# Performance work log

Measured on AMD Instinct MI355X. Metric: run time of the kernel, lower is better.

Reference implementation:

```python
import jax, jax.numpy as jnp
import numpy as np

B, T, D = 4, 4096, 1024
H = 16
DH = D // H
F = 4096
EPS = 1e-5


def _layernorm(x, gamma, beta):
    mu = jnp.mean(x, axis=-1, keepdims=True)
    var = jnp.var(x, axis=-1, keepdims=True)
    return (x - mu) * jax.lax.rsqrt(var + EPS) * gamma + beta


def setup_inputs() -> dict:
    key = jax.random.key(0)
    ks = jax.random.split(key, 10)
    s = 0.02
    return {
        "x": jax.random.normal(ks[0], (B, T, D), dtype=jnp.float32),
        "Wqkv": jax.random.normal(ks[1], (D, 3 * D), dtype=jnp.float32) * s,
        "bqkv": jnp.zeros((3 * D,), dtype=jnp.float32),
        "Wo": jax.random.normal(ks[2], (D, D), dtype=jnp.float32) * s,
        "bo": jnp.zeros((D,), dtype=jnp.float32),
        "W1": jax.random.normal(ks[3], (D, F), dtype=jnp.float32) * s,
        "b1": jnp.zeros((F,), dtype=jnp.float32),
        "W2": jax.random.normal(ks[4], (F, D), dtype=jnp.float32) * s,
        "b2": jnp.zeros((D,), dtype=jnp.float32),
        "g1": jnp.ones((D,), dtype=jnp.float32),
        "be1": jnp.zeros((D,), dtype=jnp.float32),
        "g2": jnp.ones((D,), dtype=jnp.float32),
        "be2": jnp.zeros((D,), dtype=jnp.float32),
    }


def reference(x, Wqkv, bqkv, Wo, bo, W1, b1, W2, b2, g1, be1, g2, be2):
    # fused QKV projection: [B,T,3D]
    qkv = jnp.einsum("btd,de->bte", x, Wqkv) + bqkv
    q, k, v = jnp.split(qkv, 3, axis=-1)
    # [B,H,T,DH]
    q = q.reshape(B, T, H, DH).transpose(0, 2, 1, 3)
    k = k.reshape(B, T, H, DH).transpose(0, 2, 1, 3)
    v = v.reshape(B, T, H, DH).transpose(0, 2, 1, 3)
    scores = jnp.einsum("bhqd,bhkd->bhqk", q, k) / jnp.sqrt(jnp.float32(DH))
    attn = jax.nn.softmax(scores, axis=-1)
    ctx = jnp.einsum("bhqk,bhkd->bhqd", attn, v)
    ctx = ctx.transpose(0, 2, 1, 3).reshape(B, T, D)
    # output projection + residual + post-LN
    x = _layernorm(x + (jnp.einsum("btd,de->bte", ctx, Wo) + bo), g1, be1)
    # FFN (exact GELU, torch default) + residual + post-LN
    h = jax.nn.gelu(jnp.einsum("btd,df->btf", x, W1) + b1, approximate=False)
    ffn = jnp.einsum("btf,fd->btd", h, W2) + b2
    return _layernorm(x + ffn, g2, be2)
```

## Files before the change

kernel.cpp:

```cpp
#include <hip/hip_runtime.h>
#include <math.h>

typedef unsigned short u16;
typedef unsigned int   u32;
typedef __attribute__((ext_vector_type(8))) short short8;
typedef __attribute__((ext_vector_type(4))) float f32x4;

#define B_  4
#define T_  4096
#define D_  1024
#define H_  16
#define DH_ 64
#define F_  4096
#define EPS_ 1e-5f
#define QKV_LD (3 * D_)

#define QSCALE_ 0.18033688011112042f

__device__ __forceinline__ float b2f(u16 v) {
    union { u32 u; float f; } x; x.u = ((u32)v) << 16; return x.f;
}
__device__ __forceinline__ u16 f2b(float f) {
    union { u32 u; float f; } x; x.f = f;
    u32 r = (x.u >> 16) & 1u;
    return (u16)((x.u + 0x7fffu + r) >> 16);
}
__device__ __forceinline__ u16 f2b_fast(float f) {
    union { u32 u; float f; } x; x.f = f;
    return (u16)((x.u + 0x8000u) >> 16);
}

__device__ __forceinline__ float ex2(float x) {
    float r;
    asm("v_exp_f32 %0, %1" : "=v"(r) : "v"(x));
    return r;
}

__device__ __forceinline__ void gll16(const u16* g, u16* ldsbase) {
    __builtin_amdgcn_global_load_lds(
        (const __attribute__((address_space(1))) void*)g,
        (__attribute__((address_space(3))) void*)ldsbase, 16, 0, 0);
}

__global__ __launch_bounds__(256) void conv_bf16_kernel(
    const float* __restrict__ in, u16* __restrict__ out)
{
    const int i = blockIdx.x * 256 + threadIdx.x;
    float4 v = ((const float4*)in)[i];
    ushort4 o;
    o.x = f2b(v.x); o.y = f2b(v.y); o.z = f2b(v.z); o.w = f2b(v.w);
    ((ushort4*)out)[i] = o;
}

__global__ __launch_bounds__(256) void transpose_bf16_kernel(
    const float* __restrict__ W, u16* __restrict__ Wt, int R, int C)
{
    __shared__ float tile[32][33];
    const int bx = blockIdx.x * 32;
    const int by = blockIdx.y * 32;
    const int tx = threadIdx.x & 31, ty = threadIdx.x >> 5;
#pragma unroll
    for (int p = 0; p < 4; ++p)
        tile[ty + p * 8][tx] = W[(size_t)(by + ty + p * 8) * C + bx + tx];
    __syncthreads();
#pragma unroll
    for (int p = 0; p < 4; ++p)
        Wt[(size_t)(bx + ty + p * 8) * R + by + tx] = f2b(tile[tx][ty + p * 8]);
}

template<bool CBF>
__global__ __launch_bounds__(256) void mfma_gemm(
    const u16* __restrict__ A, int lda,
    const u16* __restrict__ Bt, int ldbt,
    const float* __restrict__ bias,
    void* __restrict__ Cv, int ldc,
    int K, int act, int acc, int qcols)
{
    __shared__ __align__(16) u16 Al[128 * 32];
    __shared__ __align__(16) u16 Bl[128 * 32];

    const int tid  = threadIdx.x;
    const int lane = tid & 63, wave = tid >> 6;
    const int quad = lane >> 4, l16 = lane & 15;
    const int m0 = blockIdx.y * 128, n0 = blockIdx.x * 128;
    const int wm = (wave >> 1) * 64, wn = (wave & 1) * 64;

    int srow[2], sgk[2];
#pragma unroll
    for (int t = 0; t < 2; ++t) {
        const int c = wave * 128 + t * 64 + lane;
        srow[t] = c >> 2;
        sgk[t] = ((c & 3) ^ ((srow[t] >> 1) & 3)) * 8;
    }
    const u16* Ag = A  + (size_t)m0 * lda;
    const u16* Bg = Bt + (size_t)n0 * ldbt;
    const int apos = (quad ^ ((l16 >> 1) & 3)) * 8;

    f32x4 accr[4][4];
#pragma unroll
    for (int i = 0; i < 4; ++i)
#pragma unroll
        for (int j = 0; j < 4; ++j)
            accr[i][j] = (f32x4)(0.0f);

    for (int k0 = 0; k0 < K; k0 += 32) {
        __syncthreads();
#pragma unroll
        for (int t = 0; t < 2; ++t) {
            gll16(Ag + (size_t)srow[t] * lda  + k0 + sgk[t], &Al[(wave * 128 + t * 64) * 8]);
            gll16(Bg + (size_t)srow[t] * ldbt + k0 + sgk[t], &Bl[(wave * 128 + t * 64) * 8]);
        }
        __syncthreads();

        short8 af[4], bf[4];
#pragma unroll
        for (int i = 0; i < 4; ++i)
            af[i] = *(const short8*)&Al[(wm + i * 16 + l16) * 32 + apos];
#pragma unroll
        for (int j = 0; j < 4; ++j)
            bf[j] = *(const short8*)&Bl[(wn + j * 16 + l16) * 32 + apos];
#pragma unroll
        for (int i = 0; i < 4; ++i)
#pragma unroll
            for (int j = 0; j < 4; ++j)
                accr[i][j] = __builtin_amdgcn_mfma_f32_16x16x32_bf16(
                    af[i], bf[j], accr[i][j], 0, 0, 0);
    }

#pragma unroll
    for (int j = 0; j < 4; ++j) {
        const int cc = n0 + wn + j * 16 + l16;
        float bv = acc ? 0.0f : bias[cc];
        const float sc = (cc < qcols) ? QSCALE_ : 1.0f;
#pragma unroll
        for (int i = 0; i < 4; ++i) {
#pragma unroll
            for (int r = 0; r < 4; ++r) {
                const int rr = m0 + wm + i * 16 + quad * 4 + r;
                float v = (accr[i][j][r] + bv) * sc;
                if (act == 1)
                    v = 0.5f * v * (1.0f + erff(v * 0.70710678118654752f));
                if (CBF) {
                    ((u16*)Cv)[(size_t)rr * ldc + cc] = f2b(v);
                } else {
                    float* dst = (float*)Cv + (size_t)rr * ldc + cc;
                    if (acc) v += *dst;
                    *dst = v;
                }
            }
        }
    }
}

__global__ __launch_bounds__(256) void attn_mfma_kernel(
    const u16* __restrict__ qkv, u16* __restrict__ ctx)
{
    __shared__ u16 Ks[64 * 72];
    __shared__ u16 Vt[64 * 72];
    __shared__ u16 Ps[4][32 * 72];

    const int tid  = threadIdx.x;
    const int lane = tid & 63, wave = tid >> 6;
    const int quad = lane >> 4, l16 = lane & 15;
    const int b = blockIdx.z, h = blockIdx.y;
    const int q0 = blockIdx.x * 128;

    short8 aq[2][2];
    {
        const u16* qb = qkv + (size_t)(b * T_ + q0 + wave * 32) * QKV_LD + h * DH_;
#pragma unroll
        for (int u = 0; u < 2; ++u)
#pragma unroll
            for (int s = 0; s < 2; ++s)
                aq[u][s] = *(const short8*)(qb + (size_t)(u * 16 + l16) * QKV_LD + s * 32 + quad * 8);
    }

    const int srow = tid >> 3;
    const int scol = (tid & 7) * 8;
    const u16* kg = qkv + (size_t)(b * T_) * QKV_LD + D_     + h * DH_;
    const u16* vg = qkv + (size_t)(b * T_) * QKV_LD + 2 * D_ + h * DH_;

    short8 kreg[2], vreg[2];
#pragma unroll
    for (int half = 0; half < 2; ++half) {
        const int row = srow + half * 32;
        kreg[half] = *(const short8*)(kg + (size_t)row * QKV_LD + scol);
        vreg[half] = *(const short8*)(vg + (size_t)row * QKV_LD + scol);
    }

    f32x4 o_acc[2][4];
#pragma unroll
    for (int u = 0; u < 2; ++u)
#pragma unroll
        for (int nt = 0; nt < 4; ++nt)
            o_acc[u][nt] = (f32x4)(0.0f);
    float l_part[2][4] = {};

    for (int kt = 0; kt < T_; kt += 64) {
        __syncthreads();
#pragma unroll
        for (int half = 0; half < 2; ++half) {
            const int row = srow + half * 32;
            *(short8*)&Ks[row * 72 + scol] = kreg[half];
            u16* vd = &Vt[row ^ scol];
#pragma unroll
            for (int jj = 0; jj < 8; ++jj)
                vd[(scol + jj) * 72] = ((const u16*)&vreg[half])[jj];
        }
        __syncthreads();

        if (kt + 64 < T_) {
#pragma unroll
            for (int half = 0; half < 2; ++half) {
                const int row = srow + half * 32;
                kreg[half] = *(const short8*)(kg + (size_t)(kt + 64 + row) * QKV_LD + scol);
                vreg[half] = *(const short8*)(vg + (size_t)(kt + 64 + row) * QKV_LD + scol);
            }
        }

        f32x4 sa[2][4];
#pragma unroll
        for (int u = 0; u < 2; ++u)
#pragma unroll
            for (int nt = 0; nt < 4; ++nt)
                sa[u][nt] = (f32x4)(0.0f);
#pragma unroll
        for (int s = 0; s < 2; ++s) {
            short8 kb[4];
#pragma unroll
            for (int nt = 0; nt < 4; ++nt)
                kb[nt] = *(const short8*)&Ks[(nt * 16 + l16) * 72 + s * 32 + quad * 8];
#pragma unroll
            for (int u = 0; u < 2; ++u)
#pragma unroll
                for (int nt = 0; nt < 4; ++nt)
                    sa[u][nt] = __builtin_amdgcn_mfma_f32_16x16x32_bf16(
                        aq[u][s], kb[nt], sa[u][nt], 0, 0, 0);
        }

#pragma unroll
        for (int u = 0; u < 2; ++u) {
#pragma unroll
            for (int nt = 0; nt < 4; ++nt) {
#pragma unroll
                for (int r = 0; r < 4; ++r) {
                    float p = ex2(sa[u][nt][r]);
                    l_part[u][r] += p;
                    Ps[wave][(u * 16 + quad * 4 + r) * 72 + nt * 16 + l16] = f2b_fast(p);
                }
            }
        }

#pragma unroll
        for (int s = 0; s < 2; ++s) {
            short8 pa[2];
#pragma unroll
            for (int u = 0; u < 2; ++u)
                pa[u] = *(const short8*)&Ps[wave][(u * 16 + l16) * 72 + s * 32 + quad * 8];
#pragma unroll
            for (int nt = 0; nt < 4; ++nt) {
                const int dh = nt * 16 + l16;
                short8 vb = *(const short8*)&Vt[dh * 72 + ((s * 32 + quad * 8) ^ (dh & 56))];
#pragma unroll
                for (int u = 0; u < 2; ++u)
                    o_acc[u][nt] = __builtin_amdgcn_mfma_f32_16x16x32_bf16(
                        pa[u], vb, o_acc[u][nt], 0, 0, 0);
            }
        }
    }

#pragma unroll
    for (int u = 0; u < 2; ++u) {
#pragma unroll
        for (int r = 0; r < 4; ++r) {
            float l = l_part[u][r];
            l += __shfl_xor(l, 1, 64);
            l += __shfl_xor(l, 2, 64);
            l += __shfl_xor(l, 4, 64);
            l += __shfl_xor(l, 8, 64);
            const float inv = 1.0f / l;
            const size_t row = (size_t)(b * T_ + q0 + wave * 32 + u * 16 + quad * 4 + r);
#pragma unroll
            for (int nt = 0; nt < 4; ++nt)
                ctx[row * D_ + h * DH_ + nt * 16 + l16] = f2b(o_acc[u][nt][r] * inv);
        }
    }
}

template<bool ABF, bool BBF, bool OBF>
__global__ __launch_bounds__(256) void add_ln_kernel(
    const void* __restrict__ av, const void* __restrict__ bv,
    const float* __restrict__ g, const float* __restrict__ be,
    void* __restrict__ outv)
{
    const int row = blockIdx.x;
    const int tid = threadIdx.x;

    float v[4];
    if (ABF) {
        ushort4 va = *(const ushort4*)((const u16*)av + (size_t)row * D_ + tid * 4);
        v[0] = b2f(va.x); v[1] = b2f(va.y); v[2] = b2f(va.z); v[3] = b2f(va.w);
    } else {
        float4 va = *(const float4*)((const float*)av + (size_t)row * D_ + tid * 4);
        v[0] = va.x; v[1] = va.y; v[2] = va.z; v[3] = va.w;
    }
    if (BBF) {
        ushort4 vb = *(const ushort4*)((const u16*)bv + (size_t)row * D_ + tid * 4);
        v[0] += b2f(vb.x); v[1] += b2f(vb.y); v[2] += b2f(vb.z); v[3] += b2f(vb.w);
    } else {
        float4 vb = *(const float4*)((const float*)bv + (size_t)row * D_ + tid * 4);
        v[0] += vb.x; v[1] += vb.y; v[2] += vb.z; v[3] += vb.w;
    }

    float s  = v[0] + v[1] + v[2] + v[3];
    float ss = v[0]*v[0] + v[1]*v[1] + v[2]*v[2] + v[3]*v[3];
#pragma unroll
    for (int off = 32; off > 0; off >>= 1) {
        s  += __shfl_down(s,  off, 64);
        ss += __shfl_down(ss, off, 64);
    }
    __shared__ float ws[4], wss[4], stats[2];
    const int wave = tid >> 6, lane = tid & 63;
    if (lane == 0) { ws[wave] = s; wss[wave] = ss; }
    __syncthreads();
    if (tid == 0) {
        float ts  = ws[0] + ws[1] + ws[2] + ws[3];
        float tss = wss[0] + wss[1] + wss[2] + wss[3];
        float mu  = ts * (1.0f / D_);
        float var = tss * (1.0f / D_) - mu * mu;
        stats[0] = mu;
        stats[1] = rsqrtf(var + EPS_);
    }
    __syncthreads();
    const float mu = stats[0], rs = stats[1];

    const float4 g4  = *(const float4*)(g  + tid * 4);
    const float4 be4 = *(const float4*)(be + tid * 4);
    float gg[4]  = {g4.x, g4.y, g4.z, g4.w};
    float beb[4] = {be4.x, be4.y, be4.z, be4.w};
    if (OBF) {
        ushort4 o;
        o.x = f2b((v[0] - mu) * rs * gg[0] + beb[0]);
        o.y = f2b((v[1] - mu) * rs * gg[1] + beb[1]);
        o.z = f2b((v[2] - mu) * rs * gg[2] + beb[2]);
        o.w = f2b((v[3] - mu) * rs * gg[3] + beb[3]);
        *(ushort4*)((u16*)outv + (size_t)row * D_ + tid * 4) = o;
    } else {
        float4 o;
        o.x = (v[0] - mu) * rs * gg[0] + beb[0];
        o.y = (v[1] - mu) * rs * gg[1] + beb[1];
        o.z = (v[2] - mu) * rs * gg[2] + beb[2];
        o.w = (v[3] - mu) * rs * gg[3] + beb[3];
        *(float4*)((float*)outv + (size_t)row * D_ + tid * 4) = o;
    }
}

extern "C" void kernel_launch(void* const* d_in, const int* in_sizes, int n_in,
                              void* d_out, int out_size, void* d_ws, size_t ws_size,
                              hipStream_t stream)
{
    const float* x    = (const float*)d_in[0];
    const float* Wqkv = (const float*)d_in[1];
    const float* bqkv = (const float*)d_in[2];
    const float* Wo   = (const float*)d_in[3];
    const float* bo   = (const float*)d_in[4];
    const float* W1   = (const float*)d_in[5];
    const float* b1   = (const float*)d_in[6];
    const float* W2   = (const float*)d_in[7];
    const float* b2   = (const float*)d_in[8];
    const float* g1   = (const float*)d_in[9];
    const float* be1  = (const float*)d_in[10];
    const float* g2   = (const float*)d_in[11];
    const float* be2  = (const float*)d_in[12];
    float* out = (float*)d_out;

    const int M = B_ * T_;
    char* ws = (char*)d_ws;
    char* sc = (char*)d_out;

    u16*   qkvB   = (u16*)ws;
    u16*   ctxB   = (u16*)(ws + (size_t)100663296);
    float* proj   = (float*)ws;
    u16*   x1B    = (u16*)(ws + (size_t)100663296);
    u16*   hchunk = (u16*)ws;
    u16*   ffnB   = (u16*)(ws + (size_t)67108864);

    u16* xB    = (u16*)sc;
    u16* WqkvT = (u16*)(sc + (size_t)33554432);
    u16* WoT   = (u16*)(sc + (size_t)39845888);
    u16* W1T   = (u16*)(sc + (size_t)41943040);
    u16* W2T   = (u16*)(sc + (size_t)50331648);

    dim3 blk(256);

    conv_bf16_kernel<<<dim3(M * D_ / 1024), blk, 0, stream>>>(x, xB);
    transpose_bf16_kernel<<<dim3(3 * D_ / 32, D_ / 32), blk, 0, stream>>>(Wqkv, WqkvT, D_, 3 * D_);
    transpose_bf16_kernel<<<dim3(D_ / 32, D_ / 32), blk, 0, stream>>>(Wo, WoT, D_, D_);
    transpose_bf16_kernel<<<dim3(F_ / 32, D_ / 32), blk, 0, stream>>>(W1, W1T, D_, F_);
    transpose_bf16_kernel<<<dim3(D_ / 32, F_ / 32), blk, 0, stream>>>(W2, W2T, F_, D_);

    mfma_gemm<true><<<dim3(3 * D_ / 128, M / 128), blk, 0, stream>>>(
        xB, D_, WqkvT, D_, bqkv, qkvB, 3 * D_, D_, 0, 0, D_);

    attn_mfma_kernel<<<dim3(T_ / 128, H_, B_), blk, 0, stream>>>(qkvB, ctxB);

    mfma_gemm<false><<<dim3(D_ / 128, M / 128), blk, 0, stream>>>(
        ctxB, D_, WoT, D_, bo, proj, D_, D_, 0, 0, 0);

    add_ln_kernel<false, false, true><<<dim3(M), blk, 0, stream>>>(x, proj, g1, be1, x1B);

    for (int mc = 0; mc < 2; ++mc) {
        const size_t m0 = (size_t)mc * 8192;
        mfma_gemm<true><<<dim3(F_ / 128, 8192 / 128), blk, 0, stream>>>(
            x1B + m0 * D_, D_, W1T, D_, b1, hchunk, F_, D_, 1, 0, 0);
        mfma_gemm<true><<<dim3(D_ / 128, 8192 / 128), blk, 0, stream>>>(
            hchunk, F_, W2T, F_, b2, ffnB + m0 * D_, D_, F_, 0, 0, 0);
    }

    add_ln_kernel<true, true, false><<<dim3(M), blk, 0, stream>>>(x1B, ffnB, g2, be2, out);
}
```

Before: 1.164 ms.

## Enlarge GEMM tiles to 256x256 with 512 threads and multi-stage LDS prefetch pipeline

The MFMA GEMM moves from 128x128 tiles with 256 threads to 256x256 tiles with 512 threads (8 waves, each computing 128x64). It also replaces the sync-load-sync loop with a 4-buffer LDS ring that prefetches two K-steps ahead using vmcnt waits, and raises wave priority around the MFMA block. The aim is more operand reuse per byte loaded and hiding global-load latency behind compute. In exchange, LDS use grows to 128 KB per block, register pressure goes up with 32 accumulators per wave, and the grid has fewer blocks, which can cut occupancy.

```diff
diff --git a/kernel.cpp b/kernel.cpp
--- a/kernel.cpp
+++ b/kernel.cpp
@@ -69,63 +69,87 @@
 }
 
 template<bool CBF>
-__global__ __launch_bounds__(256) void mfma_gemm(
+__global__ __launch_bounds__(512, 2) void mfma_gemm(
     const u16* __restrict__ A, int lda,
     const u16* __restrict__ Bt, int ldbt,
     const float* __restrict__ bias,
     void* __restrict__ Cv, int ldc,
     int K, int act, int acc, int qcols)
 {
-    __shared__ __align__(16) u16 Al[128 * 32];
-    __shared__ __align__(16) u16 Bl[128 * 32];
+    __shared__ __align__(16) u16 Al[4][256 * 32];
+    __shared__ __align__(16) u16 Bl[4][256 * 32];
 
     const int tid  = threadIdx.x;
     const int lane = tid & 63, wave = tid >> 6;
     const int quad = lane >> 4, l16 = lane & 15;
-    const int m0 = blockIdx.y * 128, n0 = blockIdx.x * 128;
-    const int wm = (wave >> 1) * 64, wn = (wave & 1) * 64;
+    const int m0 = blockIdx.y * 256, n0 = blockIdx.x * 256;
+    const int wm = (wave >> 2) * 128;
+    const int wn = (wave & 3) * 64;
 
     int srow[2], sgk[2];
 #pragma unroll
-    for (int t = 0; t < 2; ++t) {
-        const int c = wave * 128 + t * 64 + lane;
-        srow[t] = c >> 2;
-        sgk[t] = ((c & 3) ^ ((srow[t] >> 1) & 3)) * 8;
+    for (int c = 0; c < 2; ++c) {
+        srow[c] = c * 128 + wave * 16 + (lane >> 2);
+        sgk[c]  = ((lane & 3) ^ ((srow[c] >> 1) & 3)) * 8;
     }
     const u16* Ag = A  + (size_t)m0 * lda;
     const u16* Bg = Bt + (size_t)n0 * ldbt;
-    const int apos = (quad ^ ((l16 >> 1) & 3)) * 8;
-
-    f32x4 accr[4][4];
-#pragma unroll
-    for (int i = 0; i < 4; ++i)
+    const int apos  = (quad ^ ((l16 >> 1) & 3)) * 8;
+    const int ldst  = wave * 512;
+
+    f32x4 accr[8][4];
+#pragma unroll
+    for (int i = 0; i < 8; ++i)
 #pragma unroll
         for (int j = 0; j < 4; ++j)
             accr[i][j] = (f32x4)(0.0f);
 
-    for (int k0 = 0; k0 < K; k0 += 32) {
-        __syncthreads();
-#pragma unroll
-        for (int t = 0; t < 2; ++t) {
-            gll16(Ag + (size_t)srow[t] * lda  + k0 + sgk[t], &Al[(wave * 128 + t * 64) * 8]);
-            gll16(Bg + (size_t)srow[t] * ldbt + k0 + sgk[t], &Bl[(wave * 128 + t * 64) * 8]);
-        }
-        __syncthreads();
-
-        short8 af[4], bf[4];
-#pragma unroll
-        for (int i = 0; i < 4; ++i)
-            af[i] = *(const short8*)&Al[(wm + i * 16 + l16) * 32 + apos];
+    const int nt = K >> 5;
+
+#define STAGE_(t_) do {                                                        \
+        const int k0_ = (t_) * 32;                                             \
+        u16* al_ = &Al[(t_) & 3][0];                                           \
+        u16* bl_ = &Bl[(t_) & 3][0];                                           \
+        _Pragma("unroll")                                                      \
+        for (int c = 0; c < 2; ++c) {                                          \
+            gll16(Ag + (size_t)srow[c] * lda  + k0_ + sgk[c],                  \
+                  al_ + c * 4096 + ldst);                                      \
+            gll16(Bg + (size_t)srow[c] * ldbt + k0_ + sgk[c],                  \
+                  bl_ + c * 4096 + ldst);                                      \
+        }                                                                      \
+    } while (0)
+
+    STAGE_(0);
+    STAGE_(1);
+
+    for (int t = 0; t < nt; ++t) {
+        if (t + 1 < nt) asm volatile("s_waitcnt vmcnt(4)" ::: "memory");
+        else            asm volatile("s_waitcnt vmcnt(0)" ::: "memory");
+        __builtin_amdgcn_s_barrier();
+        asm volatile("" ::: "memory");
+
+        if (t + 2 < nt) STAGE_(t + 2);
+
+        const u16* al = &Al[t & 3][0];
+        const u16* bl = &Bl[t & 3][0];
+        short8 af[8], bf[4];
+#pragma unroll
+        for (int i = 0; i < 8; ++i)
+            af[i] = *(const short8*)&al[(wm + i * 16 + l16) * 32 + apos];
 #pragma unroll
         for (int j = 0; j < 4; ++j)
-            bf[j] = *(const short8*)&Bl[(wn + j * 16 + l16) * 32 + apos];
-#pragma unroll
-        for (int i = 0; i < 4; ++i)
+            bf[j] = *(const short8*)&bl[(wn + j * 16 + l16) * 32 + apos];
+
+        __builtin_amdgcn_s_setprio(1);
+#pragma unroll
+        for (int i = 0; i < 8; ++i)
 #pragma unroll
             for (int j = 0; j < 4; ++j)
                 accr[i][j] = __builtin_amdgcn_mfma_f32_16x16x32_bf16(
                     af[i], bf[j], accr[i][j], 0, 0, 0);
-    }
+        __builtin_amdgcn_s_setprio(0);
+    }
+#undef STAGE_
 
 #pragma unroll
     for (int j = 0; j < 4; ++j) {
@@ -133,7 +157,7 @@
         float bv = acc ? 0.0f : bias[cc];
         const float sc = (cc < qcols) ? QSCALE_ : 1.0f;
 #pragma unroll
-        for (int i = 0; i < 4; ++i) {
+        for (int i = 0; i < 8; ++i) {
 #pragma unroll
             for (int r = 0; r < 4; ++r) {
                 const int rr = m0 + wm + i * 16 + quad * 4 + r;
@@ -392,6 +416,7 @@
     u16* W2T   = (u16*)(sc + (size_t)50331648);
 
     dim3 blk(256);
+    dim3 gblk(512);
 
     conv_bf16_kernel<<<dim3(M * D_ / 1024), blk, 0, stream>>>(x, xB);
     transpose_bf16_kernel<<<dim3(3 * D_ / 32, D_ / 32), blk, 0, stream>>>(Wqkv, WqkvT, D_, 3 * D_);
@@ -399,21 +424,21 @@
     transpose_bf16_kernel<<<dim3(F_ / 32, D_ / 32), blk, 0, stream>>>(W1, W1T, D_, F_);
     transpose_bf16_kernel<<<dim3(D_ / 32, F_ / 32), blk, 0, stream>>>(W2, W2T, F_, D_);
 
-    mfma_gemm<true><<<dim3(3 * D_ / 128, M / 128), blk, 0, stream>>>(
+    mfma_gemm<true><<<dim3(3 * D_ / 256, M / 256), gblk, 0, stream>>>(
         xB, D_, WqkvT, D_, bqkv, qkvB, 3 * D_, D_, 0, 0, D_);
 
     attn_mfma_kernel<<<dim3(T_ / 128, H_, B_), blk, 0, stream>>>(qkvB, ctxB);
 
-    mfma_gemm<false><<<dim3(D_ / 128, M / 128), blk, 0, stream>>>(
+    mfma_gemm<false><<<dim3(D_ / 256, M / 256), gblk, 0, stream>>>(
         ctxB, D_, WoT, D_, bo, proj, D_, D_, 0, 0, 0);
 
     add_ln_kernel<false, false, true><<<dim3(M), blk, 0, stream>>>(x, proj, g1, be1, x1B);
 
     for (int mc = 0; mc < 2; ++mc) {
         const size_t m0 = (size_t)mc * 8192;
-        mfma_gemm<true><<<dim3(F_ / 128, 8192 / 128), blk, 0, stream>>>(
+        mfma_gemm<true><<<dim3(F_ / 256, 8192 / 256), gblk, 0, stream>>>(
             x1B + m0 * D_, D_, W1T, D_, b1, hchunk, F_, D_, 1, 0, 0);
-        mfma_gemm<true><<<dim3(D_ / 128, 8192 / 128), blk, 0, stream>>>(
+        mfma_gemm<true><<<dim3(D_ / 256, 8192 / 256), gblk, 0, stream>>>(
             hchunk, F_, W2T, F_, b2, ffnB + m0 * D_, D_, F_, 0, 0, 0);
     }
 
```

Result: slower. 1.249 ms (+7.3%).

## Compute softmax row sums via MFMA, add wave priority, use polynomial GELU erf

Applied to the files above, without the earlier changes.

The attention kernel now takes the softmax denominator from an extra MFMA of the bf16 probability tile against a ones vector, instead of per-lane float adds followed by a cross-lane shuffle reduction. The MFMA phases are wrapped in s_setprio so the matrix work is issued ahead of other waves. Separately, the GELU epilogue swaps erff for an Abramowitz-Stegun polynomial using hardware rcp and exp2, which cuts ALU work in the FFN GEMM epilogue. The denominator is now summed from bf16-rounded probabilities and the erf approximation has roughly 1e-7 absolute error, so numerics shift slightly.

```diff
diff --git a/kernel.cpp b/kernel.cpp
--- a/kernel.cpp
+++ b/kernel.cpp
@@ -35,6 +35,26 @@
     asm("v_exp_f32 %0, %1" : "=v"(r) : "v"(x));
     return r;
 }
+__device__ __forceinline__ float rcp_(float x) {
+    float r;
+    asm("v_rcp_f32 %0, %1" : "=v"(r) : "v"(x));
+    return r;
+}
+
+__device__ __forceinline__ float gelu_erf(float x) {
+    const float z = fabsf(x) * 0.70710678118654752f;
+    const float t = rcp_(1.0f + 0.3275911f * z);
+    float poly = 1.061405429f;
+    poly = poly * t - 1.453152027f;
+    poly = poly * t + 1.421413741f;
+    poly = poly * t - 0.284496736f;
+    poly = poly * t + 0.254829592f;
+    poly = poly * t;
+    const float e = ex2(-z * z * 1.4426950408889634f);
+    const float erfz = 1.0f - poly * e;
+    const float se = copysignf(erfz, x);
+    return 0.5f * x * (1.0f + se);
+}
 
 __device__ __forceinline__ void gll16(const u16* g, u16* ldsbase) {
     __builtin_amdgcn_global_load_lds(
@@ -139,7 +159,7 @@
                 const int rr = m0 + wm + i * 16 + quad * 4 + r;
                 float v = (accr[i][j][r] + bv) * sc;
                 if (act == 1)
-                    v = 0.5f * v * (1.0f + erff(v * 0.70710678118654752f));
+                    v = gelu_erf(v);
                 if (CBF) {
                     ((u16*)Cv)[(size_t)rr * ldc + cc] = f2b(v);
                 } else {
@@ -165,6 +185,10 @@
     const int b = blockIdx.z, h = blockIdx.y;
     const int q0 = blockIdx.x * 128;
 
+    short8 ones8;
+#pragma unroll
+    for (int i = 0; i < 8; ++i) ones8[i] = (short)0x3F80;
+
     short8 aq[2][2];
     {
         const u16* qb = qkv + (size_t)(b * T_ + q0 + wave * 32) * QKV_LD + h * DH_;
@@ -194,7 +218,9 @@
 #pragma unroll
         for (int nt = 0; nt < 4; ++nt)
             o_acc[u][nt] = (f32x4)(0.0f);
-    float l_part[2][4] = {};
+    f32x4 l_acc[2];
+    l_acc[0] = (f32x4)(0.0f);
+    l_acc[1] = (f32x4)(0.0f);
 
     for (int kt = 0; kt < T_; kt += 64) {
         __syncthreads();
@@ -224,6 +250,7 @@
 #pragma unroll
             for (int nt = 0; nt < 4; ++nt)
                 sa[u][nt] = (f32x4)(0.0f);
+        __builtin_amdgcn_s_setprio(1);
 #pragma unroll
         for (int s = 0; s < 2; ++s) {
             short8 kb[4];
@@ -237,6 +264,7 @@
                     sa[u][nt] = __builtin_amdgcn_mfma_f32_16x16x32_bf16(
                         aq[u][s], kb[nt], sa[u][nt], 0, 0, 0);
         }
+        __builtin_amdgcn_s_setprio(0);
 
 #pragma unroll
         for (int u = 0; u < 2; ++u) {
@@ -245,18 +273,22 @@
 #pragma unroll
                 for (int r = 0; r < 4; ++r) {
                     float p = ex2(sa[u][nt][r]);
-                    l_part[u][r] += p;
                     Ps[wave][(u * 16 + quad * 4 + r) * 72 + nt * 16 + l16] = f2b_fast(p);
                 }
             }
         }
 
+        __builtin_amdgcn_s_setprio(1);
 #pragma unroll
         for (int s = 0; s < 2; ++s) {
             short8 pa[2];
 #pragma unroll
             for (int u = 0; u < 2; ++u)
                 pa[u] = *(const short8*)&Ps[wave][(u * 16 + l16) * 72 + s * 32 + quad * 8];
+#pragma unroll
+            for (int u = 0; u < 2; ++u)
+                l_acc[u] = __builtin_amdgcn_mfma_f32_16x16x32_bf16(
+                    pa[u], ones8, l_acc[u], 0, 0, 0);
 #pragma unroll
             for (int nt = 0; nt < 4; ++nt) {
                 const int dh = nt * 16 + l16;
@@ -267,18 +299,14 @@
                         pa[u], vb, o_acc[u][nt], 0, 0, 0);
             }
         }
+        __builtin_amdgcn_s_setprio(0);
     }
 
 #pragma unroll
     for (int u = 0; u < 2; ++u) {
 #pragma unroll
         for (int r = 0; r < 4; ++r) {
-            float l = l_part[u][r];
-            l += __shfl_xor(l, 1, 64);
-            l += __shfl_xor(l, 2, 64);
-            l += __shfl_xor(l, 4, 64);
-            l += __shfl_xor(l, 8, 64);
-            const float inv = 1.0f / l;
+            const float inv = 1.0f / l_acc[u][r];
             const size_t row = (size_t)(b * T_ + q0 + wave * 32 + u * 16 + quad * 4 + r);
 #pragma unroll
             for (int nt = 0; nt < 4; ++nt)
```

After: 1.159 ms. About the same (-0.4%).
